# Optimization experiments

Measured on AMD Instinct MI355X. Metric: run time of the kernel, lower is better.

## Reference

```python
import jax, jax.numpy as jnp
import numpy as np

K = 3        # kernel size
STRIDE = 1
PAD = 1
DIL = 1
COUT = 128


def setup_inputs() -> dict:
    key = jax.random.key(0)
    k1, k2, k3 = jax.random.split(key, 3)
    B, C, H, W = 16, 64, 64, 64
    x = jax.random.normal(k1, (B, C, H, W), dtype=jnp.float32)
    # offset layout (DCNv1, dg=1): channels = 2*K*K, per kernel tap (dy, dx)
    offset = jax.random.normal(k2, (B, 2 * K * K, H, W), dtype=jnp.float32)
    n = C * K * K
    stdv = 1.0 / float(np.sqrt(n))
    weight = jax.random.uniform(k3, (COUT, C, K, K), dtype=jnp.float32,
                                minval=-stdv, maxval=stdv)
    return {"x": x, "offset": offset, "weight": weight}


def _bilinear_sample(x, py, px):
    """x: [B,C,H,W]; py/px: [B,K2,Ho,Wo] float sample coords.
    Returns [B,K2,Ho,Wo,C] with zero padding outside the image."""
    B, C, H, W = x.shape
    y0 = jnp.floor(py)
    x0 = jnp.floor(px)
    ly = py - y0  # fractional parts
    lx = px - x0
    bi = jnp.arange(B)[:, None, None, None]

    def samp(yf, xf):
        valid = (yf >= 0) & (yf <= H - 1) & (xf >= 0) & (xf <= W - 1)
        yc = jnp.clip(yf.astype(jnp.int32), 0, H - 1)
        xc = jnp.clip(xf.astype(jnp.int32), 0, W - 1)
        # mixed advanced indexing -> [B, K2, Ho, Wo, C]
        v = x[bi, :, yc, xc]
        return v * valid[..., None].astype(x.dtype)

    w00 = ((1 - ly) * (1 - lx))[..., None]
    w01 = ((1 - ly) * lx)[..., None]
    w10 = (ly * (1 - lx))[..., None]
    w11 = (ly * lx)[..., None]
    return (w00 * samp(y0, x0) + w01 * samp(y0, x0 + 1)
            + w10 * samp(y0 + 1, x0) + w11 * samp(y0 + 1, x0 + 1))


def reference(x, offset, weight):
    B, C, H, W = x.shape
    Ho = (H + 2 * PAD - DIL * (K - 1) - 1) // STRIDE + 1
    Wo = (W + 2 * PAD - DIL * (K - 1) - 1) // STRIDE + 1
    # offset: [B, K2, 2, Ho, Wo], channel pairs are (dy, dx) per kernel tap
    off = offset.reshape(B, K * K, 2, Ho, Wo)
    ky, kx = jnp.meshgrid(jnp.arange(K), jnp.arange(K), indexing="ij")
    ky = (ky.reshape(-1) * DIL).astype(jnp.float32)  # [K2]
    kx = (kx.reshape(-1) * DIL).astype(jnp.float32)
    base_y = (jnp.arange(Ho) * STRIDE - PAD).astype(jnp.float32)  # [Ho]
    base_x = (jnp.arange(Wo) * STRIDE - PAD).astype(jnp.float32)  # [Wo]
    py = off[:, :, 0] + base_y[None, None, :, None] + ky[None, :, None, None]
    px = off[:, :, 1] + base_x[None, None, None, :] + kx[None, :, None, None]
    col = _bilinear_sample(x, py, px)  # [B, K2, Ho, Wo, C]
    # im2col GEMM: contract over (c, k)
    w = weight.reshape(weight.shape[0], C, K * K)  # [Cout, Cin, K2]
    out = jnp.einsum("bkhwc,ock->bohw", col, w)
    return out
```

## Files before the change

kernel.cpp:

```cpp
#include <hip/hip_runtime.h>


typedef short bf8 __attribute__((ext_vector_type(8)));
typedef float f32x4 __attribute__((ext_vector_type(4)));
typedef unsigned short u16;
typedef u16 u16x8 __attribute__((ext_vector_type(8)));

__device__ inline u16 f2bf(float f) {
    unsigned u = __float_as_uint(f);
    return (u16)((u + 0x7FFFu + ((u >> 16) & 1u)) >> 16);
}
__device__ inline float bf2f(u16 v) {
    return __uint_as_float(((unsigned)v) << 16);
}

__global__ __launch_bounds__(256) void transpose_x_kernel(const float* __restrict__ x,
                                                          u16* __restrict__ xtb) {
    __shared__ float tile[64][65];
    int bid = blockIdx.x;
    int t = threadIdx.x;
    int b = bid >> 6, y = bid & 63;
    const float* xb = x + (size_t)b * 262144 + (size_t)y * 64;
#pragma unroll
    for (int it = 0; it < 16; ++it) {
        int idx = t + it * 256;
        int c = idx >> 6, w = idx & 63;
        tile[c][w] = xb[(size_t)c * 4096 + w];
    }
    __syncthreads();
    u16* dst = xtb + (size_t)bid * 4096;
#pragma unroll
    for (int it = 0; it < 16; ++it) {
        int idx = t + it * 256;
        dst[idx] = f2bf(tile[idx & 63][idx >> 6]);
    }
}

__global__ __launch_bounds__(256) void build_wfrag(const float* __restrict__ wgt,
                                                   short* __restrict__ wf) {
    int idx = blockIdx.x * 256 + threadIdx.x;
    int i = idx & 7;
    int lane = (idx >> 3) & 63;
    int ks = (idx >> 9) & 1;
    int oct = (idx >> 10) & 7;
    int kk = idx >> 13;
    int oc = oct * 16 + (lane & 15);
    int c = ks * 32 + (lane >> 4) * 8 + i;
    wf[idx] = (short)f2bf(wgt[((size_t)oc * 64 + c) * 9 + kk]);
}

__global__ __launch_bounds__(256) void deform_main(const u16* __restrict__ xtb,
                                                   const float* __restrict__ offset,
                                                   const short* __restrict__ wf,
                                                   float* __restrict__ out) {
    __shared__ __align__(16) char smem[17408];
    short* colf = (short*)smem;
    float* off_s = (float*)(smem + 8192);

    int wg = blockIdx.x;
    int wgid = (wg & 7) * 128 + (wg >> 3);
    int b = wgid >> 6, ho = wgid & 63;
    int t = threadIdx.x;
    int wave = t >> 6, lane = t & 63;

    {
        const float* ob = offset + (size_t)b * 18 * 4096 + ho * 64;
        for (int idx = t; idx < 18 * 64; idx += 256)
            off_s[idx] = ob[(idx >> 6) * 4096 + (idx & 63)];
    }
    __syncthreads();

    f32x4 acc[4][2];
#pragma unroll
    for (int m = 0; m < 4; ++m)
#pragma unroll
        for (int j = 0; j < 2; ++j) acc[m][j] = (f32x4)0.f;

    const int px = t >> 2, cq = t & 3;
    const int pxt = px >> 4, wo15 = px & 15, ks_p = cq >> 1, kgb = (cq & 1) * 2;
    const u16* xb = xtb + (size_t)b * 262144;

    for (int kk = 0; kk < 9; ++kk) {
        bf8 bfr0[2], bfr1[2];
#pragma unroll
        for (int ksi = 0; ksi < 2; ++ksi) {
            bfr0[ksi] = *(const bf8*)(wf + ((((kk * 8 + 2 * wave) * 2) + ksi) * 64 + lane) * 8);
            bfr1[ksi] = *(const bf8*)(wf + ((((kk * 8 + 2 * wave + 1) * 2) + ksi) * 64 + lane) * 8);
        }

        {
            int ky = kk / 3, kx = kk - ky * 3;
            float py = off_s[(2 * kk) * 64 + px] + (float)(ho - 1 + ky);
            float sx = off_s[(2 * kk + 1) * 64 + px] + (float)(px - 1 + kx);
            float y0f = floorf(py), x0f = floorf(sx);
            float ly = py - y0f, lx = sx - x0f;
            int y0 = (int)y0f, x0 = (int)x0f;
            int y1 = y0 + 1, x1 = x0 + 1;
            float w00 = (1.f - ly) * (1.f - lx), w01 = (1.f - ly) * lx;
            float w10 = ly * (1.f - lx), w11 = ly * lx;
            bool vy0 = (y0 >= 0) & (y0 < 64), vy1 = (y1 >= 0) & (y1 < 64);
            bool vx0 = (x0 >= 0) & (x0 < 64), vx1 = (x1 >= 0) & (x1 < 64);
            if (!(vy0 & vx0)) w00 = 0.f;
            if (!(vy0 & vx1)) w01 = 0.f;
            if (!(vy1 & vx0)) w10 = 0.f;
            if (!(vy1 & vx1)) w11 = 0.f;
            int y0c = min(max(y0, 0), 63), y1c = min(max(y1, 0), 63);
            int x0c = min(max(x0, 0), 63), x1c = min(max(x1, 0), 63);
            const u16x8* q00 = (const u16x8*)(xb + ((y0c * 64 + x0c) * 64) + cq * 16);
            const u16x8* q01 = (const u16x8*)(xb + ((y0c * 64 + x1c) * 64) + cq * 16);
            const u16x8* q10 = (const u16x8*)(xb + ((y1c * 64 + x0c) * 64) + cq * 16);
            const u16x8* q11 = (const u16x8*)(xb + ((y1c * 64 + x1c) * 64) + cq * 16);
#pragma unroll
            for (int g = 0; g < 2; ++g) {
                u16x8 a = q00[g], bb = q01[g], cc = q10[g], dd = q11[g];
                bf8 v;
#pragma unroll
                for (int i = 0; i < 8; ++i) {
                    float r = w00 * bf2f(a[i]) + w01 * bf2f(bb[i]) +
                              w10 * bf2f(cc[i]) + w11 * bf2f(dd[i]);
                    v[i] = (short)f2bf(r);
                }
                int lanew = ((kgb + g) << 4) | wo15;
                *(bf8*)(colf + ((pxt * 2 + ks_p) * 64 + lanew) * 8) = v;
            }
        }
        __syncthreads();

#pragma unroll
        for (int ksi = 0; ksi < 2; ++ksi) {
            bf8 a[4];
#pragma unroll
            for (int m = 0; m < 4; ++m)
                a[m] = *(const bf8*)(colf + ((m * 2 + ksi) * 64 + lane) * 8);
#pragma unroll
            for (int m = 0; m < 4; ++m) {
                acc[m][0] = __builtin_amdgcn_mfma_f32_16x16x32_bf16(a[m], bfr0[ksi], acc[m][0], 0, 0, 0);
                acc[m][1] = __builtin_amdgcn_mfma_f32_16x16x32_bf16(a[m], bfr1[ksi], acc[m][1], 0, 0, 0);
            }
        }
        __syncthreads();
    }

    float* ep = (float*)(smem + wave * 4352);
    float* outb = out + (size_t)b * 128 * 4096 + ho * 64;
    const int ocl = lane & 15, hi = lane >> 4;
    const int ocr = lane >> 2, px0 = (lane & 3) * 16;
#pragma unroll
    for (int j = 0; j < 2; ++j) {
#pragma unroll
        for (int m = 0; m < 4; ++m)
            *(f32x4*)(ep + ocl * 68 + m * 16 + hi * 4) = acc[m][j];
        int ocg = (2 * wave + j) * 16 + ocr;
#pragma unroll
        for (int q = 0; q < 4; ++q) {
            f32x4 v = *(const f32x4*)(ep + ocr * 68 + px0 + q * 4);
            *(f32x4*)(outb + (size_t)ocg * 4096 + px0 + q * 4) = v;
        }
    }
}

extern "C" void kernel_launch(void* const* d_in, const int* in_sizes, int n_in,
                              void* d_out, int out_size, void* d_ws, size_t ws_size,
                              hipStream_t stream) {
    const float* x = (const float*)d_in[0];
    const float* offset = (const float*)d_in[1];
    const float* wgt = (const float*)d_in[2];
    float* out = (float*)d_out;
    u16* xtb = (u16*)d_ws;
    short* wfrag = (short*)(xtb + (size_t)16 * 64 * 64 * 64);

    hipLaunchKernelGGL(transpose_x_kernel, dim3(1024), dim3(256), 0, stream, x, xtb);
    hipLaunchKernelGGL(build_wfrag, dim3(288), dim3(256), 0, stream, wgt, wfrag);
    hipLaunchKernelGGL(deform_main, dim3(1024), dim3(256), 0, stream, xtb, offset, wfrag, out);
}
```

Before: 114.2 us.

## Double-buffer im2col tile and prefetch next tap's gathers during MFMA

Adds a second LDS column buffer so that the bilinear gathers for tap kk+1 are issued into registers before the MFMAs for tap kk and interpolated afterwards. This drops one barrier per tap and hides global gather latency behind matrix work. The transpose kernel also packs two bf16 channels per 32-bit store to cut store instructions. The cost is more registers held across the MFMA section, which may lower occupancy, and a larger LDS allocation.

```diff
diff --git a/kernel.cpp b/kernel.cpp
--- a/kernel.cpp
+++ b/kernel.cpp
@@ -28,11 +28,14 @@
         tile[c][w] = xb[(size_t)c * 4096 + w];
     }
     __syncthreads();
-    u16* dst = xtb + (size_t)bid * 4096;
-#pragma unroll
-    for (int it = 0; it < 16; ++it) {
-        int idx = t + it * 256;
-        dst[idx] = f2bf(tile[idx & 63][idx >> 6]);
+    unsigned* dst = (unsigned*)(xtb + (size_t)bid * 4096);
+#pragma unroll
+    for (int it = 0; it < 8; ++it) {
+        int p = t + it * 256;
+        int w = p >> 5, c0 = (p & 31) * 2;
+        unsigned lo = f2bf(tile[c0][w]);
+        unsigned hi = f2bf(tile[c0 + 1][w]);
+        dst[p] = lo | (hi << 16);
     }
 }
 
@@ -53,9 +56,9 @@
                                                    const float* __restrict__ offset,
                                                    const short* __restrict__ wf,
                                                    float* __restrict__ out) {
-    __shared__ __align__(16) char smem[17408];
+    __shared__ __align__(16) char smem[20992];
     short* colf = (short*)smem;
-    float* off_s = (float*)(smem + 8192);
+    float* off_s = (float*)(smem + 16384);
 
     int wg = blockIdx.x;
     int wgid = (wg & 7) * 128 + (wg >> 3);
@@ -79,8 +82,64 @@
     const int px = t >> 2, cq = t & 3;
     const int pxt = px >> 4, wo15 = px & 15, ks_p = cq >> 1, kgb = (cq & 1) * 2;
     const u16* xb = xtb + (size_t)b * 262144;
+    const int cbase0 = ((pxt * 2 + ks_p) * 64 + ((kgb + 0) << 4 | wo15)) * 8;
+    const int cbase1 = ((pxt * 2 + ks_p) * 64 + ((kgb + 1) << 4 | wo15)) * 8;
+
+    u16x8 g00a, g01a, g10a, g11a, g00b, g01b, g10b, g11b;
+    float w00, w01, w10, w11;
+
+#define GATHER_ISSUE(KK)                                                        \
+    {                                                                           \
+        int ky = (KK) / 3, kx = (KK) - ky * 3;                                  \
+        float py = off_s[(2 * (KK)) * 64 + px] + (float)(ho - 1 + ky);          \
+        float sx = off_s[(2 * (KK) + 1) * 64 + px] + (float)(px - 1 + kx);      \
+        float y0f = floorf(py), x0f = floorf(sx);                               \
+        float ly = py - y0f, lx = sx - x0f;                                     \
+        int y0 = (int)y0f, x0 = (int)x0f;                                       \
+        int y1 = y0 + 1, x1 = x0 + 1;                                           \
+        w00 = (1.f - ly) * (1.f - lx); w01 = (1.f - ly) * lx;                   \
+        w10 = ly * (1.f - lx); w11 = ly * lx;                                   \
+        bool vy0 = (y0 >= 0) & (y0 < 64), vy1 = (y1 >= 0) & (y1 < 64);          \
+        bool vx0 = (x0 >= 0) & (x0 < 64), vx1 = (x1 >= 0) & (x1 < 64);          \
+        if (!(vy0 & vx0)) w00 = 0.f;                                            \
+        if (!(vy0 & vx1)) w01 = 0.f;                                            \
+        if (!(vy1 & vx0)) w10 = 0.f;                                            \
+        if (!(vy1 & vx1)) w11 = 0.f;                                            \
+        int y0c = min(max(y0, 0), 63), y1c = min(max(y1, 0), 63);               \
+        int x0c = min(max(x0, 0), 63), x1c = min(max(x1, 0), 63);               \
+        const u16x8* q00 = (const u16x8*)(xb + ((y0c * 64 + x0c) * 64) + cq * 16); \
+        const u16x8* q01 = (const u16x8*)(xb + ((y0c * 64 + x1c) * 64) + cq * 16); \
+        const u16x8* q10 = (const u16x8*)(xb + ((y1c * 64 + x0c) * 64) + cq * 16); \
+        const u16x8* q11 = (const u16x8*)(xb + ((y1c * 64 + x1c) * 64) + cq * 16); \
+        g00a = q00[0]; g01a = q01[0]; g10a = q10[0]; g11a = q11[0];             \
+        g00b = q00[1]; g01b = q01[1]; g10b = q10[1]; g11b = q11[1];             \
+    }
+
+#define INTERP_WRITE(BUF)                                                       \
+    {                                                                           \
+        short* cb = colf + (BUF) * 4096;                                        \
+        bf8 va, vb;                                                             \
+        _Pragma("unroll")                                                       \
+        for (int i = 0; i < 8; ++i) {                                           \
+            float ra = w00 * bf2f(g00a[i]) + w01 * bf2f(g01a[i]) +              \
+                       w10 * bf2f(g10a[i]) + w11 * bf2f(g11a[i]);               \
+            va[i] = (short)f2bf(ra);                                            \
+            float rb = w00 * bf2f(g00b[i]) + w01 * bf2f(g01b[i]) +              \
+                       w10 * bf2f(g10b[i]) + w11 * bf2f(g11b[i]);               \
+            vb[i] = (short)f2bf(rb);                                            \
+        }                                                                       \
+        *(bf8*)(cb + cbase0) = va;                                              \
+        *(bf8*)(cb + cbase1) = vb;                                              \
+    }
+
+    GATHER_ISSUE(0);
+    INTERP_WRITE(0);
+    __syncthreads();
 
     for (int kk = 0; kk < 9; ++kk) {
+        int cur = kk & 1, nxt = cur ^ 1;
+        if (kk < 8) GATHER_ISSUE(kk + 1);
+
         bf8 bfr0[2], bfr1[2];
 #pragma unroll
         for (int ksi = 0; ksi < 2; ++ksi) {
@@ -88,58 +147,25 @@
             bfr1[ksi] = *(const bf8*)(wf + ((((kk * 8 + 2 * wave + 1) * 2) + ksi) * 64 + lane) * 8);
         }
 
-        {
-            int ky = kk / 3, kx = kk - ky * 3;
-            float py = off_s[(2 * kk) * 64 + px] + (float)(ho - 1 + ky);
-            float sx = off_s[(2 * kk + 1) * 64 + px] + (float)(px - 1 + kx);
-            float y0f = floorf(py), x0f = floorf(sx);
-            float ly = py - y0f, lx = sx - x0f;
-            int y0 = (int)y0f, x0 = (int)x0f;
-            int y1 = y0 + 1, x1 = x0 + 1;
-            float w00 = (1.f - ly) * (1.f - lx), w01 = (1.f - ly) * lx;
-            float w10 = ly * (1.f - lx), w11 = ly * lx;
-            bool vy0 = (y0 >= 0) & (y0 < 64), vy1 = (y1 >= 0) & (y1 < 64);
-            bool vx0 = (x0 >= 0) & (x0 < 64), vx1 = (x1 >= 0) & (x1 < 64);
-            if (!(vy0 & vx0)) w00 = 0.f;
-            if (!(vy0 & vx1)) w01 = 0.f;
-            if (!(vy1 & vx0)) w10 = 0.f;
-            if (!(vy1 & vx1)) w11 = 0.f;
-            int y0c = min(max(y0, 0), 63), y1c = min(max(y1, 0), 63);
-            int x0c = min(max(x0, 0), 63), x1c = min(max(x1, 0), 63);
-            const u16x8* q00 = (const u16x8*)(xb + ((y0c * 64 + x0c) * 64) + cq * 16);
-            const u16x8* q01 = (const u16x8*)(xb + ((y0c * 64 + x1c) * 64) + cq * 16);
-            const u16x8* q10 = (const u16x8*)(xb + ((y1c * 64 + x0c) * 64) + cq * 16);
-            const u16x8* q11 = (const u16x8*)(xb + ((y1c * 64 + x1c) * 64) + cq * 16);
-#pragma unroll
-            for (int g = 0; g < 2; ++g) {
-                u16x8 a = q00[g], bb = q01[g], cc = q10[g], dd = q11[g];
-                bf8 v;
-#pragma unroll
-                for (int i = 0; i < 8; ++i) {
-                    float r = w00 * bf2f(a[i]) + w01 * bf2f(bb[i]) +
-                              w10 * bf2f(cc[i]) + w11 * bf2f(dd[i]);
-                    v[i] = (short)f2bf(r);
-                }
-                int lanew = ((kgb + g) << 4) | wo15;
-                *(bf8*)(colf + ((pxt * 2 + ks_p) * 64 + lanew) * 8) = v;
-            }
-        }
-        __syncthreads();
-
+        const short* cb = colf + cur * 4096;
 #pragma unroll
         for (int ksi = 0; ksi < 2; ++ksi) {
             bf8 a[4];
 #pragma unroll
             for (int m = 0; m < 4; ++m)
-                a[m] = *(const bf8*)(colf + ((m * 2 + ksi) * 64 + lane) * 8);
+                a[m] = *(const bf8*)(cb + ((m * 2 + ksi) * 64 + lane) * 8);
 #pragma unroll
             for (int m = 0; m < 4; ++m) {
                 acc[m][0] = __builtin_amdgcn_mfma_f32_16x16x32_bf16(a[m], bfr0[ksi], acc[m][0], 0, 0, 0);
                 acc[m][1] = __builtin_amdgcn_mfma_f32_16x16x32_bf16(a[m], bfr1[ksi], acc[m][1], 0, 0, 0);
             }
         }
+
+        if (kk < 8) INTERP_WRITE(nxt);
         __syncthreads();
     }
+#undef GATHER_ISSUE
+#undef INTERP_WRITE
 
     float* ep = (float*)(smem + wave * 4352);
     float* outb = out + (size_t)b * 128 * 4096 + ho * 64;
```

New measurement: 114.3 us. Within noise of the previous version (+0.1%).

## Restructure deform conv into single-wave blocks with register-resident A fragments

Applied to the files above, without the earlier changes.

The main kernel now launches 4096 one-wave blocks, each covering 16 output pixels and all 128 output channels. Each lane builds its bilinear-sampled A fragments directly in registers, which removes the shared-memory column staging and the two barriers per tap. The cost is that every wave loads all weight fragments for each tap (16 bf8 loads), weight reuse across pixels drops, and the epilogue adds barriers per output group. The transpose kernel also packs two bf16 values into each 32-bit store.

```diff
diff --git a/kernel.cpp b/kernel.cpp
--- a/kernel.cpp
+++ b/kernel.cpp
@@ -28,11 +28,14 @@
         tile[c][w] = xb[(size_t)c * 4096 + w];
     }
     __syncthreads();
-    u16* dst = xtb + (size_t)bid * 4096;
+    unsigned* dst = (unsigned*)(xtb + (size_t)bid * 4096);
 #pragma unroll
-    for (int it = 0; it < 16; ++it) {
-        int idx = t + it * 256;
-        dst[idx] = f2bf(tile[idx & 63][idx >> 6]);
+    for (int it = 0; it < 8; ++it) {
+        int p = t + it * 256;
+        int w = p >> 5, c0 = (p & 31) * 2;
+        unsigned lo = f2bf(tile[c0][w]);
+        unsigned hi = f2bf(tile[c0 + 1][w]);
+        dst[p] = lo | (hi << 16);
     }
 }
 
@@ -49,113 +52,100 @@
     wf[idx] = (short)f2bf(wgt[((size_t)oc * 64 + c) * 9 + kk]);
 }
 
-__global__ __launch_bounds__(256) void deform_main(const u16* __restrict__ xtb,
-                                                   const float* __restrict__ offset,
-                                                   const short* __restrict__ wf,
-                                                   float* __restrict__ out) {
-    __shared__ __align__(16) char smem[17408];
-    short* colf = (short*)smem;
-    float* off_s = (float*)(smem + 8192);
+__global__ __launch_bounds__(64, 4) void deform_main(const u16* __restrict__ xtb,
+                                                     const float* __restrict__ offset,
+                                                     const short* __restrict__ wf,
+                                                     float* __restrict__ out) {
+    __shared__ float off_lds[288];
+    __shared__ __align__(16) float eps[320];
 
     int wg = blockIdx.x;
-    int wgid = (wg & 7) * 128 + (wg >> 3);
-    int b = wgid >> 6, ho = wgid & 63;
-    int t = threadIdx.x;
-    int wave = t >> 6, lane = t & 63;
+    int wgid = (wg & 7) * 512 + (wg >> 3);
+    int b = wgid >> 8, ho = (wgid >> 2) & 63, px0 = (wgid & 3) << 4;
+    int l = threadIdx.x;
+    const int pxl = l & 15;
+    const int c0 = (l >> 4) * 8;
 
     {
-        const float* ob = offset + (size_t)b * 18 * 4096 + ho * 64;
-        for (int idx = t; idx < 18 * 64; idx += 256)
-            off_s[idx] = ob[(idx >> 6) * 4096 + (idx & 63)];
+        const float* ob = offset + (size_t)b * 73728 + ho * 64 + px0;
+        for (int idx = l; idx < 288; idx += 64)
+            off_lds[idx] = ob[(idx >> 4) * 4096 + (idx & 15)];
     }
     __syncthreads();
 
-    f32x4 acc[4][2];
+    f32x4 acc[8];
 #pragma unroll
-    for (int m = 0; m < 4; ++m)
-#pragma unroll
-        for (int j = 0; j < 2; ++j) acc[m][j] = (f32x4)0.f;
+    for (int o = 0; o < 8; ++o) acc[o] = (f32x4)0.f;
 
-    const int px = t >> 2, cq = t & 3;
-    const int pxt = px >> 4, wo15 = px & 15, ks_p = cq >> 1, kgb = (cq & 1) * 2;
     const u16* xb = xtb + (size_t)b * 262144;
+    const float fpx = (float)(px0 + pxl - 1);
 
     for (int kk = 0; kk < 9; ++kk) {
-        bf8 bfr0[2], bfr1[2];
+        int ky = kk / 3, kx = kk - ky * 3;
+        float py = off_lds[(2 * kk) * 16 + pxl] + (float)(ho - 1 + ky);
+        float sx = off_lds[(2 * kk + 1) * 16 + pxl] + fpx + (float)kx;
+        float y0f = floorf(py), x0f = floorf(sx);
+        float ly = py - y0f, lx = sx - x0f;
+        int y0 = (int)y0f, x0 = (int)x0f;
+        int y1 = y0 + 1, x1 = x0 + 1;
+        float w00 = (1.f - ly) * (1.f - lx), w01 = (1.f - ly) * lx;
+        float w10 = ly * (1.f - lx), w11 = ly * lx;
+        bool vy0 = (y0 >= 0) & (y0 < 64), vy1 = (y1 >= 0) & (y1 < 64);
+        bool vx0 = (x0 >= 0) & (x0 < 64), vx1 = (x1 >= 0) & (x1 < 64);
+        if (!(vy0 & vx0)) w00 = 0.f;
+        if (!(vy0 & vx1)) w01 = 0.f;
+        if (!(vy1 & vx0)) w10 = 0.f;
+        if (!(vy1 & vx1)) w11 = 0.f;
+        int y0c = min(max(y0, 0), 63), y1c = min(max(y1, 0), 63);
+        int x0c = min(max(x0, 0), 63), x1c = min(max(x1, 0), 63);
+
+        const u16* p00 = xb + ((y0c * 64 + x0c) * 64) + c0;
+        const u16* p01 = xb + ((y0c * 64 + x1c) * 64) + c0;
+        const u16* p10 = xb + ((y1c * 64 + x0c) * 64) + c0;
+        const u16* p11 = xb + ((y1c * 64 + x1c) * 64) + c0;
+        u16x8 g00a = *(const u16x8*)p00,        g00b = *(const u16x8*)(p00 + 32);
+        u16x8 g01a = *(const u16x8*)p01,        g01b = *(const u16x8*)(p01 + 32);
+        u16x8 g10a = *(const u16x8*)p10,        g10b = *(const u16x8*)(p10 + 32);
+        u16x8 g11a = *(const u16x8*)p11,        g11b = *(const u16x8*)(p11 + 32);
+
+        bf8 af0, af1;
 #pragma unroll
-        for (int ksi = 0; ksi < 2; ++ksi) {
-            bfr0[ksi] = *(const bf8*)(wf + ((((kk * 8 + 2 * wave) * 2) + ksi) * 64 + lane) * 8);
-            bfr1[ksi] = *(const bf8*)(wf + ((((kk * 8 + 2 * wave + 1) * 2) + ksi) * 64 + lane) * 8);
+        for (int i = 0; i < 8; ++i) {
+            float ra = w00 * bf2f(g00a[i]) + w01 * bf2f(g01a[i]) +
+                       w10 * bf2f(g10a[i]) + w11 * bf2f(g11a[i]);
+            af0[i] = (short)f2bf(ra);
+            float rb = w00 * bf2f(g00b[i]) + w01 * bf2f(g01b[i]) +
+                       w10 * bf2f(g10b[i]) + w11 * bf2f(g11b[i]);
+            af1[i] = (short)f2bf(rb);
         }
 
-        {
-            int ky = kk / 3, kx = kk - ky * 3;
-            float py = off_s[(2 * kk) * 64 + px] + (float)(ho - 1 + ky);
-            float sx = off_s[(2 * kk + 1) * 64 + px] + (float)(px - 1 + kx);
-            float y0f = floorf(py), x0f = floorf(sx);
-            float ly = py - y0f, lx = sx - x0f;
-            int y0 = (int)y0f, x0 = (int)x0f;
-            int y1 = y0 + 1, x1 = x0 + 1;
-            float w00 = (1.f - ly) * (1.f - lx), w01 = (1.f - ly) * lx;
-            float w10 = ly * (1.f - lx), w11 = ly * lx;
-            bool vy0 = (y0 >= 0) & (y0 < 64), vy1 = (y1 >= 0) & (y1 < 64);
-            bool vx0 = (x0 >= 0) & (x0 < 64), vx1 = (x1 >= 0) & (x1 < 64);
-            if (!(vy0 & vx0)) w00 = 0.f;
-            if (!(vy0 & vx1)) w01 = 0.f;
-            if (!(vy1 & vx0)) w10 = 0.f;
-            if (!(vy1 & vx1)) w11 = 0.f;
-            int y0c = min(max(y0, 0), 63), y1c = min(max(y1, 0), 63);
-            int x0c = min(max(x0, 0), 63), x1c = min(max(x1, 0), 63);
-            const u16x8* q00 = (const u16x8*)(xb + ((y0c * 64 + x0c) * 64) + cq * 16);
-            const u16x8* q01 = (const u16x8*)(xb + ((y0c * 64 + x1c) * 64) + cq * 16);
-            const u16x8* q10 = (const u16x8*)(xb + ((y1c * 64 + x0c) * 64) + cq * 16);
-            const u16x8* q11 = (const u16x8*)(xb + ((y1c * 64 + x1c) * 64) + cq * 16);
+        const short* wk = wf + (size_t)kk * 8192;
+        bf8 bv[16];
 #pragma unroll
-            for (int g = 0; g < 2; ++g) {
-                u16x8 a = q00[g], bb = q01[g], cc = q10[g], dd = q11[g];
-                bf8 v;
+        for (int o = 0; o < 8; ++o) {
+            bv[2 * o]     = *(const bf8*)(wk + ((o * 2 + 0) * 64 + l) * 8);
+            bv[2 * o + 1] = *(const bf8*)(wk + ((o * 2 + 1) * 64 + l) * 8);
+        }
 #pragma unroll
-                for (int i = 0; i < 8; ++i) {
-                    float r = w00 * bf2f(a[i]) + w01 * bf2f(bb[i]) +
-                              w10 * bf2f(cc[i]) + w11 * bf2f(dd[i]);
-                    v[i] = (short)f2bf(r);
-                }
-                int lanew = ((kgb + g) << 4) | wo15;
-                *(bf8*)(colf + ((pxt * 2 + ks_p) * 64 + lanew) * 8) = v;
-            }
-        }
-        __syncthreads();
-
+        for (int o = 0; o < 8; ++o)
+            acc[o] = __builtin_amdgcn_mfma_f32_16x16x32_bf16(af0, bv[2 * o], acc[o], 0, 0, 0);
 #pragma unroll
-        for (int ksi = 0; ksi < 2; ++ksi) {
-            bf8 a[4];
-#pragma unroll
-            for (int m = 0; m < 4; ++m)
-                a[m] = *(const bf8*)(colf + ((m * 2 + ksi) * 64 + lane) * 8);
-#pragma unroll
-            for (int m = 0; m < 4; ++m) {
-                acc[m][0] = __builtin_amdgcn_mfma_f32_16x16x32_bf16(a[m], bfr0[ksi], acc[m][0], 0, 0, 0);
-                acc[m][1] = __builtin_amdgcn_mfma_f32_16x16x32_bf16(a[m], bfr1[ksi], acc[m][1], 0, 0, 0);
-            }
-        }
-        __syncthreads();
+        for (int o = 0; o < 8; ++o)
+            acc[o] = __builtin_amdgcn_mfma_f32_16x16x32_bf16(af1, bv[2 * o + 1], acc[o], 0, 0, 0);
     }
 
-    float* ep = (float*)(smem + wave * 4352);
-    float* outb = out + (size_t)b * 128 * 4096 + ho * 64;
-    const int ocl = lane & 15, hi = lane >> 4;
-    const int ocr = lane >> 2, px0 = (lane & 3) * 16;
+    float* outb = out + (size_t)b * 524288 + ho * 64 + px0;
+    const int ocw = l & 15, hiw = (l >> 4) * 4;
+    const int ocr = l >> 2, ch4 = (l & 3) * 4;
 #pragma unroll
-    for (int j = 0; j < 2; ++j) {
+    for (int o = 0; o < 8; ++o) {
 #pragma unroll
-        for (int m = 0; m < 4; ++m)
-            *(f32x4*)(ep + ocl * 68 + m * 16 + hi * 4) = acc[m][j];
-        int ocg = (2 * wave + j) * 16 + ocr;
-#pragma unroll
-        for (int q = 0; q < 4; ++q) {
-            f32x4 v = *(const f32x4*)(ep + ocr * 68 + px0 + q * 4);
-            *(f32x4*)(outb + (size_t)ocg * 4096 + px0 + q * 4) = v;
-        }
+        for (int r = 0; r < 4; ++r)
+            eps[ocw * 20 + hiw + r] = acc[o][r];
+        __syncthreads();
+        f32x4 v = *(const f32x4*)(eps + ocr * 20 + ch4);
+        *(f32x4*)(outb + (size_t)(o * 16 + ocr) * 4096 + ch4) = v;
+        __syncthreads();
     }
 }
 
@@ -171,5 +161,5 @@
 
     hipLaunchKernelGGL(transpose_x_kernel, dim3(1024), dim3(256), 0, stream, x, xtb);
     hipLaunchKernelGGL(build_wfrag, dim3(288), dim3(256), 0, stream, wgt, wfrag);
-    hipLaunchKernelGGL(deform_main, dim3(1024), dim3(256), 0, stream, xtb, offset, wfrag, out);
+    hipLaunchKernelGGL(deform_main, dim3(4096), dim3(64), 0, stream, xtb, offset, wfrag, out);
 }
```

New measurement: 135.3 us. 1.18x slower.
